# Kernel tuning notes

Measured on AMD Instinct MI355X. Metric: run time of the kernel, lower is better.

Reference implementation:

```python
import jax, jax.numpy as jnp
import numpy as np

B, I, H = 16384, 512, 512


def setup_inputs() -> dict:
    key = jax.random.key(0)
    ks = jax.random.split(key, 6)
    scale_s = 1.0 / np.sqrt(H + I + 1)
    scale_g = 1.0 / np.sqrt(H + I + H)
    return {
        "x_t": jax.random.normal(ks[0], (B, I), dtype=jnp.float32),
        "delta_t": jax.random.uniform(ks[1], (B, 1), dtype=jnp.float32),
        "h_prev": jax.random.normal(ks[2], (B, H), dtype=jnp.float32),
        "c_prev": jax.random.normal(ks[3], (B, H), dtype=jnp.float32),
        # linear_s: in = H + I + 1
        "Ws": jax.random.normal(ks[4], (H + I + 1, H), dtype=jnp.float32) * scale_s,
        "bs": jnp.zeros((H,), dtype=jnp.float32),
        # stacked weights for the 5 gates (f, i, T, u, o), each in = H + I + H
        "Wg": jax.random.normal(ks[5], (2 * H + I, 5 * H), dtype=jnp.float32) * scale_g,
        "bg": jnp.zeros((5 * H,), dtype=jnp.float32),
    }


def reference(x_t, delta_t, h_prev, c_prev, Ws, bs, Wg, bg):
    # time gate: s_t = tanh(Linear([h_prev, x_t, delta_t]))
    s_t = jnp.tanh(jnp.concatenate([h_prev, x_t, delta_t], axis=1) @ Ws + bs)
    # shared-input GEMM for the 5 gates on concat([h_prev, x_t, s_t])
    z = jnp.concatenate([h_prev, x_t, s_t], axis=1) @ Wg + bg  # [B, 5H]
    f_t = jax.nn.sigmoid(z[:, 0 * H:1 * H])
    i_t = jax.nn.sigmoid(z[:, 1 * H:2 * H])
    T_t = jax.nn.sigmoid(z[:, 2 * H:3 * H])
    zeta_t = jnp.tanh(z[:, 3 * H:4 * H])
    o_t = jax.nn.sigmoid(z[:, 4 * H:5 * H])
    c_t = f_t * c_prev + i_t * zeta_t + T_t * s_t
    h_t = o_t * jnp.tanh(c_t)
    return (h_t, c_t)
```

## Files before the change

### kernel.cpp

```cpp
#include <hip/hip_runtime.h>
#include <stdint.h>
#include <stddef.h>

#define Bsz 16384
#define Hsz 512
#define KG 1536
#define KA 1024
#define NT3 48

typedef float f32x4 __attribute__((ext_vector_type(4)));
typedef short bf16x8 __attribute__((ext_vector_type(8)));
typedef unsigned short u16;
typedef unsigned int u32;

__device__ __forceinline__ u16 f2bf(float f) {
  union { float f; unsigned u; } v; v.f = f;
  return (u16)((v.u + 0x7fffu + ((v.u >> 16) & 1u)) >> 16);
}
__device__ __forceinline__ float bf2f(u16 h) {
  union { unsigned u; float f; } v; v.u = ((unsigned)h) << 16;
  return v.f;
}
__device__ __forceinline__ float sigm(float x) {
  return 1.0f / (1.0f + __expf(-x));
}
__device__ __forceinline__ float tanh_(float x) {
  x = fminf(fmaxf(x, -15.0f), 15.0f);
  float e = __expf(2.0f * x);
  return (e - 1.0f) / (e + 1.0f);
}

__device__ __forceinline__ void gload_lds16(const u16* g, u16* l) {
  __builtin_amdgcn_global_load_lds(
      (__attribute__((address_space(1))) void*)(g),
      (__attribute__((address_space(3))) void*)(l), 16, 0, 0);
}

#define VMCNT(n) asm volatile("s_waitcnt vmcnt(" #n ")" ::: "memory")
#define BAR() { asm volatile("" ::: "memory"); __builtin_amdgcn_s_barrier(); \
                asm volatile("" ::: "memory"); }

__global__ __launch_bounds__(256) void prep_A_kernel(
    const float* __restrict__ h_prev, const float* __restrict__ x_t,
    u16* __restrict__ A) {
  const int b = blockIdx.x;
  const int q = threadIdx.x;
  const int qq = q & 127;
  const float4* src = (q < 128) ? (const float4*)h_prev : (const float4*)x_t;
  float4 v = src[(size_t)b * 128 + qq];
  ushort4 o;
  o.x = f2bf(v.x); o.y = f2bf(v.y); o.z = f2bf(v.z); o.w = f2bf(v.w);
  *(ushort4*)(A + (size_t)b * KG + (size_t)q * 4) = o;
}

__global__ __launch_bounds__(256) void transpose_cast_kernel(
    const float* __restrict__ in, u16* __restrict__ out, int R, int C) {
  __shared__ float tile[32][33];
  const int c0 = blockIdx.x * 32;
  const int r0 = blockIdx.y * 32;
  const int tx = threadIdx.x;
  const int ty = threadIdx.y;
  #pragma unroll
  for (int i = ty; i < 32; i += 8)
    tile[i][tx] = in[(size_t)(r0 + i) * C + (c0 + tx)];
  __syncthreads();
  #pragma unroll
  for (int i = ty; i < 32; i += 8)
    out[(size_t)(c0 + i) * R + (r0 + tx)] = f2bf(tile[tx][i]);
}

__global__ __launch_bounds__(256, 2) void gemm1_kernel(
    const u16* __restrict__ A, const u16* __restrict__ Wst,
    const float* __restrict__ Ws, const float* __restrict__ bs,
    const float* __restrict__ delta, u16* __restrict__ Aout) {
  __shared__ __attribute__((aligned(16))) u16 Als[128][32];
  __shared__ __attribute__((aligned(16))) u16 Bls[128][32];
  const int t = threadIdx.x;
  const int w = t >> 6, l = t & 63;
  const int bm0 = blockIdx.y * 128;
  const int bn0 = blockIdx.x * 128;
  const int wm = w >> 1, wn = w & 1;

  f32x4 zv = {0.f, 0.f, 0.f, 0.f};
  f32x4 acc[4][4];
  #pragma unroll
  for (int i = 0; i < 4; ++i)
    #pragma unroll
    for (int j = 0; j < 4; ++j) acc[i][j] = zv;

  const int r = t >> 2, q = t & 3;
  const u16* gA0 = A + (size_t)(bm0 + r) * KG + q * 8;
  const u16* gA1 = A + (size_t)(bm0 + 64 + r) * KG + q * 8;
  const u16* gB0 = Wst + (size_t)(bn0 + r) * KA + q * 8;
  const u16* gB1 = Wst + (size_t)(bn0 + 64 + r) * KA + q * 8;
  u16* lA0 = &Als[0][0] + w * 512;
  u16* lA1 = &Als[0][0] + 2048 + w * 512;
  u16* lB0 = &Bls[0][0] + w * 512;
  u16* lB1 = &Bls[0][0] + 2048 + w * 512;

  const int frow = l & 15;
  const int kofs = (l >> 4) * 8;

  for (int kt = 0; kt < KA / 32; ++kt) {
    const int ko = kt * 32;
    gload_lds16(gA0 + ko, lA0);
    gload_lds16(gA1 + ko, lA1);
    gload_lds16(gB0 + ko, lB0);
    gload_lds16(gB1 + ko, lB1);
    __syncthreads();
    bf16x8 af[4], bfv[4];
    #pragma unroll
    for (int mi = 0; mi < 4; ++mi)
      af[mi] = *(const bf16x8*)&Als[wm * 64 + mi * 16 + frow][kofs];
    #pragma unroll
    for (int ni = 0; ni < 4; ++ni)
      bfv[ni] = *(const bf16x8*)&Bls[wn * 64 + ni * 16 + frow][kofs];
    #pragma unroll
    for (int mi = 0; mi < 4; ++mi)
      #pragma unroll
      for (int ni = 0; ni < 4; ++ni)
        acc[mi][ni] = __builtin_amdgcn_mfma_f32_16x16x32_bf16(
            af[mi], bfv[ni], acc[mi][ni], 0, 0, 0);
    __syncthreads();
  }

  #pragma unroll
  for (int ni = 0; ni < 4; ++ni) {
    const int col = bn0 + wn * 64 + ni * 16 + (l & 15);
    const float wsl = Ws[(size_t)1024 * 512 + col];
    const float bsv = bs[col];
    #pragma unroll
    for (int mi = 0; mi < 4; ++mi) {
      #pragma unroll
      for (int rr = 0; rr < 4; ++rr) {
        const int row = bm0 + wm * 64 + mi * 16 + (l >> 4) * 4 + rr;
        const float z = acc[mi][ni][rr] + delta[row] * wsl + bsv;
        Aout[(size_t)row * KG + 1024 + col] = f2bf(tanh_(z));
      }
    }
  }
}

__global__ __launch_bounds__(512, 2) void gemm2_p(
    const u16* __restrict__ A, const u16* __restrict__ Wgt,
    const float* __restrict__ bg, const float* __restrict__ c_prev,
    float* __restrict__ out) {
  __shared__ __attribute__((aligned(16))) u16 LDSA[3][256 * 32];
  __shared__ __attribute__((aligned(16))) u16 LDSB[3][320 * 32];

  const int t5 = threadIdx.x;
  const int w = t5 >> 6;
  const int l = t5 & 63;

  const int bid = blockIdx.x;
  const int hb = bid & 7;
  const int rb = bid >> 3;
  const int bm0 = rb * 256;
  const int h0 = hb * 64;

  const bool isA = (w < 4);

  const u16* gs0 = nullptr; const u16* gs1 = nullptr; const u16* gs2 = nullptr;
  const u16* gs3 = nullptr; const u16* gs4 = nullptr;
  u32 lo0 = 0, lo1 = 0, lo2 = 0, lo3 = 0, lo4 = 0;

  if (isA) {
#define MKA(s, gp, lo) { int idx = w * 256 + (s) * 64 + l; int row = idx >> 2; \
    int ch = (idx & 3) ^ ((idx >> 3) & 3); \
    gp = A + (size_t)(bm0 + row) * KG + ch * 8; lo = (u32)(w * 256 + (s) * 64) * 8; }
    MKA(0, gs0, lo0) MKA(1, gs1, lo1) MKA(2, gs2, lo2) MKA(3, gs3, lo3)
#undef MKA
  } else {
#define MKB(s, gp, lo) { int idx = (w - 4) * 320 + (s) * 64 + l; int rbw = idx >> 2; \
    int ch = (idx & 3) ^ ((idx >> 3) & 3); \
    int g = rbw >> 6; int hl = rbw & 63; \
    gp = Wgt + (size_t)(g * Hsz + h0 + hl) * KG + ch * 8; \
    lo = (u32)((w - 4) * 320 + (s) * 64) * 8; }
    MKB(0, gs0, lo0) MKB(1, gs1, lo1) MKB(2, gs2, lo2) MKB(3, gs3, lo3) MKB(4, gs4, lo4)
#undef MKB
  }

#define STAGE_CH0(kt, bb) { \
    if (isA) { \
      gload_lds16(gs0 + (size_t)(kt) * 32, &LDSA[bb][lo0]); \
      gload_lds16(gs1 + (size_t)(kt) * 32, &LDSA[bb][lo1]); \
    } else { \
      gload_lds16(gs0 + (size_t)(kt) * 32, &LDSB[bb][lo0]); \
      gload_lds16(gs1 + (size_t)(kt) * 32, &LDSB[bb][lo1]); \
      gload_lds16(gs2 + (size_t)(kt) * 32, &LDSB[bb][lo2]); \
    } }
#define STAGE_CH1(kt, bb) { \
    if (isA) { \
      gload_lds16(gs2 + (size_t)(kt) * 32, &LDSA[bb][lo2]); \
      gload_lds16(gs3 + (size_t)(kt) * 32, &LDSA[bb][lo3]); \
    } else { \
      gload_lds16(gs3 + (size_t)(kt) * 32, &LDSB[bb][lo3]); \
      gload_lds16(gs4 + (size_t)(kt) * 32, &LDSB[bb][lo4]); \
    } }

  f32x4 zv = {0.f, 0.f, 0.f, 0.f};
  f32x4 acc[8][5];
  #pragma unroll
  for (int mi = 0; mi < 8; ++mi)
    #pragma unroll
    for (int g = 0; g < 5; ++g) acc[mi][g] = zv;

  const int wm = w >> 2;
  const int wn = w & 3;
  const int frow = l & 15;
  const int kq = l >> 4;
  const u32 axor = (u32)((kq ^ ((frow >> 1) & 3)) << 3);
  const u32 abase = (u32)(wm * 128 + frow) * 32 + axor;
  const u32 bbase = (u32)(wn * 16 + frow) * 32 + axor;

#define LDA4(Asrc, off) { af[0] = *(const bf16x8*)&Asrc[(off)]; \
    af[1] = *(const bf16x8*)&Asrc[(off) + 512]; \
    af[2] = *(const bf16x8*)&Asrc[(off) + 1024]; \
    af[3] = *(const bf16x8*)&Asrc[(off) + 1536]; }
#define LDB5(Bsrc, off) { bfv[0] = *(const bf16x8*)&Bsrc[(off)]; \
    bfv[1] = *(const bf16x8*)&Bsrc[(off) + 2048]; \
    bfv[2] = *(const bf16x8*)&Bsrc[(off) + 4096]; \
    bfv[3] = *(const bf16x8*)&Bsrc[(off) + 6144]; \
    bfv[4] = *(const bf16x8*)&Bsrc[(off) + 8192]; }
#define MFMA20(base) { __builtin_amdgcn_s_setprio(1); \
    _Pragma("unroll") \
    for (int g = 0; g < 5; ++g) { \
      _Pragma("unroll") \
      for (int mi = 0; mi < 4; ++mi) \
        acc[(base) + mi][g] = __builtin_amdgcn_mfma_f32_16x16x32_bf16( \
            af[mi], bfv[g], acc[(base) + mi][g], 0, 0, 0); \
    } \
    __builtin_amdgcn_s_setprio(0); }

  STAGE_CH0(0, 0) STAGE_CH1(0, 0)
  STAGE_CH0(1, 1) STAGE_CH1(1, 1)

  int bt = 0;
  int bt2 = 2;
  for (int t = 0; t < NT3; ++t) {
    const int rem = NT3 - 1 - t;
    if (rem >= 1) { if (isA) { VMCNT(4); } else { VMCNT(5); } }
    else { VMCNT(0); }
    BAR();
    const u16* As = &LDSA[bt][0];
    const u16* Bs = &LDSB[bt][0];
    bf16x8 af[4], bfv[5];
    LDA4(As, abase)
    LDB5(Bs, bbase)
    if (rem >= 2) STAGE_CH0(t + 2, bt2)
    BAR();
    MFMA20(0)
    BAR();
    LDA4(As, abase + 2048)
    if (rem >= 2) STAGE_CH1(t + 2, bt2)
    BAR();
    MFMA20(4)
    bt = (bt == 2) ? 0 : bt + 1;
    bt2 = (bt2 == 2) ? 0 : bt2 + 1;
  }
#undef STAGE_CH0
#undef STAGE_CH1

  const int hc = h0 + wn * 16 + frow;
  const float b_f = bg[hc];
  const float b_i = bg[Hsz + hc];
  const float b_T = bg[2 * Hsz + hc];
  const float b_z = bg[3 * Hsz + hc];
  const float b_o = bg[4 * Hsz + hc];
  #pragma unroll
  for (int mi = 0; mi < 8; ++mi) {
    #pragma unroll
    for (int rr = 0; rr < 4; ++rr) {
      const int row = bm0 + wm * 128 + mi * 16 + kq * 4 + rr;
      const float fg = sigm(acc[mi][0][rr] + b_f);
      const float ig = sigm(acc[mi][1][rr] + b_i);
      const float Tg = sigm(acc[mi][2][rr] + b_T);
      const float zg = tanh_(acc[mi][3][rr] + b_z);
      const float og = sigm(acc[mi][4][rr] + b_o);
      const float cp = c_prev[(size_t)row * Hsz + hc];
      const float st = bf2f(A[(size_t)row * KG + 1024 + hc]);
      const float c = fg * cp + ig * zg + Tg * st;
      const float h = og * tanh_(c);
      out[(size_t)row * Hsz + hc] = h;
      out[(size_t)Bsz * Hsz + (size_t)row * Hsz + hc] = c;
    }
  }
}

extern "C" void kernel_launch(void* const* d_in, const int* in_sizes, int n_in,
                              void* d_out, int out_size, void* d_ws, size_t ws_size,
                              hipStream_t stream) {
  const float* x_t    = (const float*)d_in[0];
  const float* delta  = (const float*)d_in[1];
  const float* h_prev = (const float*)d_in[2];
  const float* c_prev = (const float*)d_in[3];
  const float* Ws     = (const float*)d_in[4];
  const float* bs     = (const float*)d_in[5];
  const float* Wg     = (const float*)d_in[6];
  const float* bg     = (const float*)d_in[7];
  float* out = (float*)d_out;

  char* wsb = (char*)d_ws;
  u16* A   = (u16*)(wsb);
  u16* Wst = (u16*)(wsb + (size_t)50331648);
  u16* Wgt = (u16*)(wsb + (size_t)51380224);

  prep_A_kernel<<<dim3(16384), dim3(256), 0, stream>>>(h_prev, x_t, A);
  transpose_cast_kernel<<<dim3(16, 32), dim3(32, 8), 0, stream>>>(Ws, Wst, 1024, 512);
  transpose_cast_kernel<<<dim3(80, 48), dim3(32, 8), 0, stream>>>(Wg, Wgt, 1536, 2560);
  gemm1_kernel<<<dim3(4, 128), dim3(256), 0, stream>>>(A, Wst, Ws, bs, delta, A);
  gemm2_p<<<dim3(512), dim3(512), 0, stream>>>(A, Wgt, bg, c_prev, out);
}
```

Before: 200.8 us.

## Cut main-loop barriers to one per K-step and issue explicit LDS reads

The GEMM2 main loop now has a single barrier per K-tile instead of four. All of a wave's global→LDS prefetch loads for tile t+2 are issued together, and the fragments are read with inline ds_read_b128 plus an explicit lgkmcnt wait. The second A half is read after the first MFMA batch without a barrier, which relies on the triple-buffer distance for correctness. The aim is less barrier stall time and more overlap between MFMA and loads. The cost is tighter reliance on hand-placed waitcnts and scheduling barriers.

```diff
diff --git a/kernel.cpp b/kernel.cpp
--- a/kernel.cpp
+++ b/kernel.cpp
@@ -36,7 +36,15 @@
       (__attribute__((address_space(3))) void*)(l), 16, 0, 0);
 }
 
+__device__ __forceinline__ bf16x8 ds_read128(u32 byte_addr) {
+  bf16x8 r;
+  asm volatile("ds_read_b128 %0, %1" : "=v"(r) : "v"(byte_addr));
+  return r;
+}
+
 #define VMCNT(n) asm volatile("s_waitcnt vmcnt(" #n ")" ::: "memory")
+#define LGKM0() { asm volatile("s_waitcnt lgkmcnt(0)" ::: "memory"); \
+                  __builtin_amdgcn_sched_barrier(0); }
 #define BAR() { asm volatile("" ::: "memory"); __builtin_amdgcn_s_barrier(); \
                 asm volatile("" ::: "memory"); }
 
@@ -141,7 +149,7 @@
   }
 }
 
-__global__ __launch_bounds__(512, 2) void gemm2_p(
+__global__ __launch_bounds__(512, 2) void gemm2_pl(
     const u16* __restrict__ A, const u16* __restrict__ Wgt,
     const float* __restrict__ bg, const float* __restrict__ c_prev,
     float* __restrict__ out) {
@@ -180,20 +188,16 @@
 #undef MKB
   }
 
-#define STAGE_CH0(kt, bb) { \
+#define STAGE(kt, bb) { \
     if (isA) { \
       gload_lds16(gs0 + (size_t)(kt) * 32, &LDSA[bb][lo0]); \
       gload_lds16(gs1 + (size_t)(kt) * 32, &LDSA[bb][lo1]); \
+      gload_lds16(gs2 + (size_t)(kt) * 32, &LDSA[bb][lo2]); \
+      gload_lds16(gs3 + (size_t)(kt) * 32, &LDSA[bb][lo3]); \
     } else { \
       gload_lds16(gs0 + (size_t)(kt) * 32, &LDSB[bb][lo0]); \
       gload_lds16(gs1 + (size_t)(kt) * 32, &LDSB[bb][lo1]); \
       gload_lds16(gs2 + (size_t)(kt) * 32, &LDSB[bb][lo2]); \
-    } }
-#define STAGE_CH1(kt, bb) { \
-    if (isA) { \
-      gload_lds16(gs2 + (size_t)(kt) * 32, &LDSA[bb][lo2]); \
-      gload_lds16(gs3 + (size_t)(kt) * 32, &LDSA[bb][lo3]); \
-    } else { \
       gload_lds16(gs3 + (size_t)(kt) * 32, &LDSB[bb][lo3]); \
       gload_lds16(gs4 + (size_t)(kt) * 32, &LDSB[bb][lo4]); \
     } }
@@ -210,30 +214,22 @@
   const int frow = l & 15;
   const int kq = l >> 4;
   const u32 axor = (u32)((kq ^ ((frow >> 1) & 3)) << 3);
-  const u32 abase = (u32)(wm * 128 + frow) * 32 + axor;
-  const u32 bbase = (u32)(wn * 16 + frow) * 32 + axor;
-
-#define LDA4(Asrc, off) { af[0] = *(const bf16x8*)&Asrc[(off)]; \
-    af[1] = *(const bf16x8*)&Asrc[(off) + 512]; \
-    af[2] = *(const bf16x8*)&Asrc[(off) + 1024]; \
-    af[3] = *(const bf16x8*)&Asrc[(off) + 1536]; }
-#define LDB5(Bsrc, off) { bfv[0] = *(const bf16x8*)&Bsrc[(off)]; \
-    bfv[1] = *(const bf16x8*)&Bsrc[(off) + 2048]; \
-    bfv[2] = *(const bf16x8*)&Bsrc[(off) + 4096]; \
-    bfv[3] = *(const bf16x8*)&Bsrc[(off) + 6144]; \
-    bfv[4] = *(const bf16x8*)&Bsrc[(off) + 8192]; }
-#define MFMA20(base) { __builtin_amdgcn_s_setprio(1); \
+  const u32 abyte = ((u32)(wm * 128 + frow) * 32 + axor) * 2;
+  const u32 bbyte = ((u32)(wn * 16 + frow) * 32 + axor) * 2;
+  const u32 ldsA0 = (u32)(uintptr_t)&LDSA[0][0];
+  const u32 ldsB0 = (u32)(uintptr_t)&LDSB[0][0];
+
+#define MFMA20(base, FR) { \
     _Pragma("unroll") \
     for (int g = 0; g < 5; ++g) { \
       _Pragma("unroll") \
       for (int mi = 0; mi < 4; ++mi) \
         acc[(base) + mi][g] = __builtin_amdgcn_mfma_f32_16x16x32_bf16( \
-            af[mi], bfv[g], acc[(base) + mi][g], 0, 0, 0); \
-    } \
-    __builtin_amdgcn_s_setprio(0); }
-
-  STAGE_CH0(0, 0) STAGE_CH1(0, 0)
-  STAGE_CH0(1, 1) STAGE_CH1(1, 1)
+            FR[mi], bfv[g], acc[(base) + mi][g], 0, 0, 0); \
+    } }
+
+  STAGE(0, 0)
+  STAGE(1, 1)
 
   int bt = 0;
   int bt2 = 2;
@@ -242,24 +238,35 @@
     if (rem >= 1) { if (isA) { VMCNT(4); } else { VMCNT(5); } }
     else { VMCNT(0); }
     BAR();
-    const u16* As = &LDSA[bt][0];
-    const u16* Bs = &LDSB[bt][0];
-    bf16x8 af[4], bfv[5];
-    LDA4(As, abase)
-    LDB5(Bs, bbase)
-    if (rem >= 2) STAGE_CH0(t + 2, bt2)
-    BAR();
-    MFMA20(0)
-    BAR();
-    LDA4(As, abase + 2048)
-    if (rem >= 2) STAGE_CH1(t + 2, bt2)
-    BAR();
-    MFMA20(4)
+    const u32 aB = ldsA0 + (u32)bt * 16384 + abyte;
+    const u32 bB = ldsB0 + (u32)bt * 20480 + bbyte;
+    bf16x8 af[4], ag[4], bfv[5];
+    af[0] = ds_read128(aB);
+    af[1] = ds_read128(aB + 1024);
+    af[2] = ds_read128(aB + 2048);
+    af[3] = ds_read128(aB + 3072);
+    bfv[0] = ds_read128(bB);
+    bfv[1] = ds_read128(bB + 4096);
+    bfv[2] = ds_read128(bB + 8192);
+    bfv[3] = ds_read128(bB + 12288);
+    bfv[4] = ds_read128(bB + 16384);
+    if (rem >= 2) STAGE(t + 2, bt2)
+    LGKM0();
+    __builtin_amdgcn_s_setprio(1);
+    MFMA20(0, af)
+    __builtin_amdgcn_s_setprio(0);
+    ag[0] = ds_read128(aB + 4096);
+    ag[1] = ds_read128(aB + 5120);
+    ag[2] = ds_read128(aB + 6144);
+    ag[3] = ds_read128(aB + 7168);
+    LGKM0();
+    __builtin_amdgcn_s_setprio(1);
+    MFMA20(4, ag)
+    __builtin_amdgcn_s_setprio(0);
     bt = (bt == 2) ? 0 : bt + 1;
     bt2 = (bt2 == 2) ? 0 : bt2 + 1;
   }
-#undef STAGE_CH0
-#undef STAGE_CH1
+#undef STAGE
 
   const int hc = h0 + wn * 16 + frow;
   const float b_f = bg[hc];
@@ -309,5 +316,5 @@
   transpose_cast_kernel<<<dim3(16, 32), dim3(32, 8), 0, stream>>>(Ws, Wst, 1024, 512);
   transpose_cast_kernel<<<dim3(80, 48), dim3(32, 8), 0, stream>>>(Wg, Wgt, 1536, 2560);
   gemm1_kernel<<<dim3(4, 128), dim3(256), 0, stream>>>(A, Wst, Ws, bs, delta, A);
-  gemm2_p<<<dim3(512), dim3(512), 0, stream>>>(A, Wgt, bg, c_prev, out);
-}
+  gemm2_pl<<<dim3(512), dim3(512), 0, stream>>>(A, Wgt, bg, c_prev, out);
+}
```

Result: no change. 201.4 us (+0.3%).
